# Optimization experiments

Hardware: AMD Instinct MI355X
Metric: run time of the kernel (lower is better)

## Reference

```python
import jax, jax.numpy as jnp
import numpy as np

N_NODES = 50000
N_EDGES = 600000
IN_FEATS = 128
H_FEATS = 128
NUM_CLASSES = 64


def setup_inputs() -> dict:
    key = jax.random.key(0)
    k = jax.random.split(key, 8)
    x = jax.random.normal(k[0], (N_NODES, IN_FEATS), dtype=jnp.float32)
    W1 = jax.random.normal(k[1], (IN_FEATS, H_FEATS), dtype=jnp.float32) * (1.0 / np.sqrt(IN_FEATS))
    b1 = jnp.zeros((H_FEATS,), dtype=jnp.float32)
    W2 = jax.random.normal(k[2], (H_FEATS, NUM_CLASSES), dtype=jnp.float32) * (1.0 / np.sqrt(H_FEATS))
    b2 = jnp.zeros((NUM_CLASSES,), dtype=jnp.float32)
    src = jax.random.randint(k[3], (N_EDGES,), 0, N_NODES, dtype=jnp.int64)
    dst = jax.random.randint(k[4], (N_EDGES,), 0, N_NODES, dtype=jnp.int64)
    return {"x": x, "W1": W1, "b1": b1, "W2": W2, "b2": b2, "src": src, "dst": dst}


def _graph_conv(h, W, b, src, dst, norm_src, norm_dst, n_nodes):
    # DGL GraphConv, norm='both': scale by 1/sqrt(out_deg(src)), sum over edges,
    # scale by 1/sqrt(in_deg(dst)), then linear transform.
    h = h * norm_src[:, None]                                   # [N, F]
    m = jax.ops.segment_sum(h[src], dst, num_segments=n_nodes)  # [N, F] scatter-add over edges
    m = m * norm_dst[:, None]
    return m @ W + b


def reference(x, W1, b1, W2, b2, src, dst):
    n = x.shape[0]
    ones = jnp.ones(src.shape[0], dtype=x.dtype)
    deg_out = jax.ops.segment_sum(ones, src, num_segments=n)
    deg_in = jax.ops.segment_sum(ones, dst, num_segments=n)
    norm_src = jax.lax.rsqrt(jnp.maximum(deg_out, 1.0))
    norm_dst = jax.lax.rsqrt(jnp.maximum(deg_in, 1.0))
    h = _graph_conv(x, W1, b1, src, dst, norm_src, norm_dst, n)
    h = jax.nn.relu(h)
    out = _graph_conv(h, W2, b2, src, dst, norm_src, norm_dst, n)
    return out
```

## Files before the change

### kernel.cpp

```cpp
#include <hip/hip_runtime.h>
#include <hip/hip_fp16.h>

#define NN 50000
#define NE 600000
#define KF 128
#define OC1 128
#define OC2 64

#define HBLK 128
#define HCH ((NE + HBLK - 1) / HBLK)
#define HP4 (NN / 4)
#define NSCB 49
#define NGB ((NN + 63) / 64)

typedef _Float16 half8 __attribute__((ext_vector_type(8)));
typedef float floatx4 __attribute__((ext_vector_type(4)));

__launch_bounds__(256)
__global__ void wt_hist_kernel(const float* __restrict__ W1, const float* __restrict__ W2,
                               __half* __restrict__ Wt1, __half* __restrict__ Wt2,
                               const int* __restrict__ src, const int* __restrict__ dst,
                               int* __restrict__ Hs, int* __restrict__ Hd) {
    __shared__ int bins[HP4];
    if (blockIdx.x < 96) {
        int i = blockIdx.x * 256 + threadIdx.x;
        if (i < KF * OC1) {
            int k = i >> 7, c = i & (OC1 - 1);
            Wt1[c * KF + k] = __float2half(W1[i]);
        } else {
            int j = i - KF * OC1;
            int k = j >> 6, c = j & (OC2 - 1);
            Wt2[c * KF + k] = __float2half(W2[j]);
        }
        return;
    }
    const int b = blockIdx.x - 96;
    const bool is_src = (b < HBLK);
    const int bb = is_src ? b : b - HBLK;
    const int* key = is_src ? src : dst;
    int* H = is_src ? Hs : Hd;
    const int e0 = bb * HCH;
    const int e1 = min(e0 + HCH, NE);

    for (int i = threadIdx.x; i < HP4; i += 256) bins[i] = 0;
    __syncthreads();
    for (int e = e0 + threadIdx.x; e < e1; e += 256) {
        int v = key[e];
        atomicAdd(&bins[v >> 2], 1 << ((v & 3) * 8));
    }
    __syncthreads();
    int* o = H + (size_t)bb * HP4;
    for (int i = threadIdx.x; i < HP4; i += 256) o[i] = bins[i];
}

__launch_bounds__(256)
__global__ void rednorm_kernel(const int* __restrict__ Hs, const int* __restrict__ Hd,
                               int* __restrict__ deg_i, float* __restrict__ nsrc,
                               float* __restrict__ ndst, int* __restrict__ bsum) {
    __shared__ int red[256];
    const int tid = threadIdx.x;
    const int p = blockIdx.x * 256 + tid;
    int so0 = 0, so1 = 0, so2 = 0, so3 = 0, si0 = 0, si1 = 0, si2 = 0, si3 = 0;
    if (p < HP4) {
#pragma unroll 4
        for (int b = 0; b < HBLK; b++) {
            int hs = Hs[(size_t)b * HP4 + p];
            int hd = Hd[(size_t)b * HP4 + p];
            so0 += hs & 255; so1 += (hs >> 8) & 255; so2 += (hs >> 16) & 255; so3 += (hs >> 24) & 255;
            si0 += hd & 255; si1 += (hd >> 8) & 255; si2 += (hd >> 16) & 255; si3 += (hd >> 24) & 255;
        }
        reinterpret_cast<int4*>(deg_i)[p] = make_int4(si0, si1, si2, si3);
        reinterpret_cast<float4*>(nsrc)[p] =
            make_float4(rsqrtf(fmaxf((float)so0, 1.f)), rsqrtf(fmaxf((float)so1, 1.f)),
                        rsqrtf(fmaxf((float)so2, 1.f)), rsqrtf(fmaxf((float)so3, 1.f)));
        reinterpret_cast<float4*>(ndst)[p] =
            make_float4(rsqrtf(fmaxf((float)si0, 1.f)), rsqrtf(fmaxf((float)si1, 1.f)),
                        rsqrtf(fmaxf((float)si2, 1.f)), rsqrtf(fmaxf((float)si3, 1.f)));
    }
    red[tid] = si0 + si1 + si2 + si3;
    __syncthreads();
    for (int off = 128; off > 0; off >>= 1) {
        if (tid < off) red[tid] += red[tid + off];
        __syncthreads();
    }
    if (tid == 0) bsum[blockIdx.x] = red[0];
}

__launch_bounds__(256)
__global__ void scanbofs_kernel(const int* __restrict__ deg, const int* __restrict__ bsum,
                                const int* __restrict__ Hd, int* __restrict__ ptr,
                                unsigned int* __restrict__ Bofs) {
    if (blockIdx.x < NSCB) {
        __shared__ int s[256];
        __shared__ int sboff;
        const int tid = threadIdx.x;
        if (tid < 64) {
            int v = (tid < (int)blockIdx.x) ? bsum[tid] : 0;
#pragma unroll
            for (int off = 32; off > 0; off >>= 1) v += __shfl_xor(v, off);
            if (tid == 0) sboff = v;
        }
        const int q = blockIdx.x * 256 + tid;
        int4 d = make_int4(0, 0, 0, 0);
        if (q < HP4) d = reinterpret_cast<const int4*>(deg)[q];
        int t4 = d.x + d.y + d.z + d.w;
        s[tid] = t4;
        __syncthreads();
        for (int off = 1; off < 256; off <<= 1) {
            int t = (tid >= off) ? s[tid - off] : 0;
            __syncthreads();
            s[tid] += t;
            __syncthreads();
        }
        if (q < HP4) {
            int base = sboff + s[tid] - t4;
            int4 pv;
            pv.x = base;
            pv.y = base + d.x;
            pv.z = pv.y + d.y;
            pv.w = pv.z + d.z;
            reinterpret_cast<int4*>(ptr)[q] = pv;
        }
        if (blockIdx.x == 0 && tid == 0) ptr[NN] = NE;
    } else {
        int p = (blockIdx.x - NSCB) * 256 + threadIdx.x;
        if (p >= HP4) return;
        int r0 = 0, r1 = 0, r2 = 0, r3 = 0;
        for (int b = 0; b < HBLK; b++) {
            Bofs[(size_t)b * HP4 + p] =
                (unsigned)(r0 | (r1 << 8) | (r2 << 16) | (r3 << 24));
            int h = Hd[(size_t)b * HP4 + p];
            r0 += h & 255; r1 += (h >> 8) & 255; r2 += (h >> 16) & 255; r3 += (h >> 24) & 255;
        }
    }
}

__launch_bounds__(256)
__global__ void fillgemm_kernel(const int* __restrict__ src, const int* __restrict__ dst,
                                const unsigned int* __restrict__ Bofs,
                                const int* __restrict__ ptr, int* __restrict__ esrc,
                                const float* __restrict__ x, const __half* __restrict__ Wt1,
                                const float* __restrict__ nsrc, __half* __restrict__ g) {
    extern __shared__ char smem[];
    if (blockIdx.x < HBLK) {
        int* cnt = (int*)smem;
        const int b = blockIdx.x;
        const int e0 = b * HCH;
        const int e1 = min(e0 + HCH, NE);
        for (int i = threadIdx.x; i < HP4; i += 256) cnt[i] = 0;
        __syncthreads();
        const unsigned char* B = (const unsigned char*)(Bofs + (size_t)b * HP4);
        for (int e = e0 + threadIdx.x; e < e1; e += 256) {
            int v = dst[e];
            int sh = (v & 3) * 8;
            int old = atomicAdd(&cnt[v >> 2], 1 << sh);
            int idx = (old >> sh) & 255;
            esrc[ptr[v] + (int)B[v] + idx] = src[e];
        }
        return;
    }
    constexpr int NT = OC1 / 16;
    constexpr int LDK = KF + 8;
    _Float16* Wsh = (_Float16*)smem;

    const int tid = threadIdx.x;
    const int wave = tid >> 6;
    const int lane = tid & 63;
    const int l16 = lane & 15;
    const int koff = (lane >> 4) * 8;
    const int row0 = (blockIdx.x - HBLK) * 64;
    const int arow = row0 + wave * 16 + l16;

    for (int i = tid; i < OC1 * (KF / 8); i += 256) {
        int r = i >> 4;
        int c8 = i & 15;
        *reinterpret_cast<uint4*>(&Wsh[r * LDK + c8 * 8]) =
            reinterpret_cast<const uint4*>(Wt1 + (size_t)r * KF)[c8];
    }

    half8 afr[4];
    if (arow < NN) {
        const float* ap = x + (size_t)arow * KF + koff;
#pragma unroll
        for (int kk = 0; kk < 4; kk++) {
            float4 v0 = *reinterpret_cast<const float4*>(ap + kk * 32);
            float4 v1 = *reinterpret_cast<const float4*>(ap + kk * 32 + 4);
            half8 h;
            h[0] = (_Float16)v0.x; h[1] = (_Float16)v0.y;
            h[2] = (_Float16)v0.z; h[3] = (_Float16)v0.w;
            h[4] = (_Float16)v1.x; h[5] = (_Float16)v1.y;
            h[6] = (_Float16)v1.z; h[7] = (_Float16)v1.w;
            afr[kk] = h;
        }
    } else {
#pragma unroll
        for (int kk = 0; kk < 4; kk++) afr[kk] = (half8)(_Float16)0;
    }

    __syncthreads();

    floatx4 acc[NT];
#pragma unroll
    for (int n = 0; n < NT; n++) acc[n] = (floatx4)(0.f);

#pragma unroll
    for (int n = 0; n < NT; n++) {
        const int brow = n * 16 + l16;
#pragma unroll
        for (int kk = 0; kk < 4; kk++) {
            half8 bfr = *reinterpret_cast<const half8*>(&Wsh[brow * LDK + kk * 32 + koff]);
            acc[n] = __builtin_amdgcn_mfma_f32_16x16x32_f16(afr[kk], bfr, acc[n], 0, 0, 0);
        }
    }

    const int crow = row0 + wave * 16 + (lane >> 4) * 4;
    float nsv[4];
#pragma unroll
    for (int j = 0; j < 4; j++) {
        int rr = crow + j;
        nsv[j] = (rr < NN) ? nsrc[rr] : 0.f;
    }
#pragma unroll
    for (int n = 0; n < NT; n++) {
#pragma unroll
        for (int j = 0; j < 4; j++) {
            int rr = crow + j;
            if (rr < NN)
                g[(size_t)rr * OC1 + n * 16 + l16] = __float2half(acc[n][j] * nsv[j]);
        }
    }
}

__launch_bounds__(256)
__global__ void gathergemm2_kernel(const __half* __restrict__ g, const int* __restrict__ ptr,
                                   const int* __restrict__ esrc, const float* __restrict__ ndst,
                                   const float* __restrict__ nsrc, const float* __restrict__ b1,
                                   const __half* __restrict__ Wt2, __half* __restrict__ g2) {
    constexpr int LDK = KF + 8;
    __shared__ _Float16 h1sh[64 * LDK];
    __shared__ _Float16 Wsh[OC2 * LDK];

    const int tid = threadIdx.x;
    const int node0 = blockIdx.x * 64;

    for (int i = tid; i < OC2 * (KF / 8); i += 256) {
        int r = i >> 4;
        int c8 = i & 15;
        *reinterpret_cast<uint4*>(&Wsh[r * LDK + c8 * 8]) =
            reinterpret_cast<const uint4*>(Wt2 + (size_t)r * KF)[c8];
    }

    const int qw = tid >> 4;
    const int l16g = tid & 15;
    const float4 bb0 = *reinterpret_cast<const float4*>(b1 + l16g * 8);
    const float4 bb1 = *reinterpret_cast<const float4*>(b1 + l16g * 8 + 4);
#pragma unroll 1
    for (int i = 0; i < 4; i++) {
        const int ln = qw + 16 * i;
        const int n = node0 + ln;
        if (n >= NN) continue;
        const int lo = ptr[n];
        const int hi = ptr[n + 1];
        const float nd = ndst[n];
        float4 a0 = make_float4(0.f, 0.f, 0.f, 0.f);
        float4 a1 = make_float4(0.f, 0.f, 0.f, 0.f);
        int e = lo;
        for (; e + 7 < hi; e += 8) {
            int s[8];
#pragma unroll
            for (int j = 0; j < 8; j++) s[j] = esrc[e + j];
            uint4 u[8];
#pragma unroll
            for (int j = 0; j < 8; j++)
                u[j] = *reinterpret_cast<const uint4*>(g + (size_t)s[j] * 128 + l16g * 8);
#pragma unroll
            for (int j = 0; j < 8; j++) {
                float2 f0 = __half22float2(*reinterpret_cast<__half2*>(&u[j].x));
                float2 f1 = __half22float2(*reinterpret_cast<__half2*>(&u[j].y));
                float2 f2 = __half22float2(*reinterpret_cast<__half2*>(&u[j].z));
                float2 f3 = __half22float2(*reinterpret_cast<__half2*>(&u[j].w));
                a0.x += f0.x; a0.y += f0.y; a0.z += f1.x; a0.w += f1.y;
                a1.x += f2.x; a1.y += f2.y; a1.z += f3.x; a1.w += f3.y;
            }
        }
        for (; e < hi; e++) {
            uint4 u = *reinterpret_cast<const uint4*>(g + (size_t)esrc[e] * 128 + l16g * 8);
            float2 f0 = __half22float2(*reinterpret_cast<__half2*>(&u.x));
            float2 f1 = __half22float2(*reinterpret_cast<__half2*>(&u.y));
            float2 f2 = __half22float2(*reinterpret_cast<__half2*>(&u.z));
            float2 f3 = __half22float2(*reinterpret_cast<__half2*>(&u.w));
            a0.x += f0.x; a0.y += f0.y; a0.z += f1.x; a0.w += f1.y;
            a1.x += f2.x; a1.y += f2.y; a1.z += f3.x; a1.w += f3.y;
        }
        const float ns = nsrc[n];
        float o0 = ns * fmaxf(fmaf(a0.x, nd, bb0.x), 0.f);
        float o1 = ns * fmaxf(fmaf(a0.y, nd, bb0.y), 0.f);
        float o2 = ns * fmaxf(fmaf(a0.z, nd, bb0.z), 0.f);
        float o3 = ns * fmaxf(fmaf(a0.w, nd, bb0.w), 0.f);
        float o4 = ns * fmaxf(fmaf(a1.x, nd, bb1.x), 0.f);
        float o5 = ns * fmaxf(fmaf(a1.y, nd, bb1.y), 0.f);
        float o6 = ns * fmaxf(fmaf(a1.z, nd, bb1.z), 0.f);
        float o7 = ns * fmaxf(fmaf(a1.w, nd, bb1.w), 0.f);
        __half2 h0 = __floats2half2_rn(o0, o1);
        __half2 h1v = __floats2half2_rn(o2, o3);
        __half2 h2 = __floats2half2_rn(o4, o5);
        __half2 h3 = __floats2half2_rn(o6, o7);
        uint4 pk;
        pk.x = *reinterpret_cast<unsigned int*>(&h0);
        pk.y = *reinterpret_cast<unsigned int*>(&h1v);
        pk.z = *reinterpret_cast<unsigned int*>(&h2);
        pk.w = *reinterpret_cast<unsigned int*>(&h3);
        *reinterpret_cast<uint4*>(&h1sh[ln * LDK + l16g * 8]) = pk;
    }
    __syncthreads();

    const int wave = tid >> 6;
    const int lane = tid & 63;
    const int l16 = lane & 15;
    const int koff = (lane >> 4) * 8;
    const int arow = wave * 16 + l16;

    half8 afr[4];
#pragma unroll
    for (int kk = 0; kk < 4; kk++)
        afr[kk] = *reinterpret_cast<const half8*>(&h1sh[arow * LDK + kk * 32 + koff]);

    floatx4 acc[4];
#pragma unroll
    for (int n = 0; n < 4; n++) acc[n] = (floatx4)(0.f);

#pragma unroll
    for (int n = 0; n < 4; n++) {
        const int brow = n * 16 + l16;
#pragma unroll
        for (int kk = 0; kk < 4; kk++) {
            half8 bfr = *reinterpret_cast<const half8*>(&Wsh[brow * LDK + kk * 32 + koff]);
            acc[n] = __builtin_amdgcn_mfma_f32_16x16x32_f16(afr[kk], bfr, acc[n], 0, 0, 0);
        }
    }

    const int crow = wave * 16 + (lane >> 4) * 4;
#pragma unroll
    for (int n = 0; n < 4; n++) {
#pragma unroll
        for (int j = 0; j < 4; j++) {
            int rr = node0 + crow + j;
            if (rr < NN)
                g2[(size_t)rr * OC2 + n * 16 + l16] = __float2half(acc[n][j]);
        }
    }
}

__launch_bounds__(256)
__global__ void gather64_kernel(const __half* __restrict__ g, const int* __restrict__ ptr,
                                const int* __restrict__ esrc, const float* __restrict__ ndst,
                                const float* __restrict__ bias, float* __restrict__ out) {
    const int node = blockIdx.x * 32 + (threadIdx.x >> 3);
    if (node >= NN) return;
    const int l8 = threadIdx.x & 7;
    const int cofs = l8 * 8;
    const int lo = ptr[node];
    const int hi = ptr[node + 1];
    const float nd = ndst[node];

    float4 ax[8], ay[8];
#pragma unroll
    for (int i = 0; i < 8; i++) {
        ax[i] = make_float4(0.f, 0.f, 0.f, 0.f);
        ay[i] = make_float4(0.f, 0.f, 0.f, 0.f);
    }

    int e = lo;
    for (; e + 7 < hi; e += 8) {
        int s[8];
#pragma unroll
        for (int i = 0; i < 8; i++) s[i] = esrc[e + i];
#pragma unroll
        for (int i = 0; i < 8; i++) {
            uint4 u = *reinterpret_cast<const uint4*>(g + (size_t)s[i] * 64 + cofs);
            float2 f0 = __half22float2(*reinterpret_cast<__half2*>(&u.x));
            float2 f1 = __half22float2(*reinterpret_cast<__half2*>(&u.y));
            float2 f2 = __half22float2(*reinterpret_cast<__half2*>(&u.z));
            float2 f3 = __half22float2(*reinterpret_cast<__half2*>(&u.w));
            ax[i].x += f0.x; ax[i].y += f0.y; ax[i].z += f1.x; ax[i].w += f1.y;
            ay[i].x += f2.x; ay[i].y += f2.y; ay[i].z += f3.x; ay[i].w += f3.y;
        }
    }
    for (; e < hi; e++) {
        uint4 u = *reinterpret_cast<const uint4*>(g + (size_t)esrc[e] * 64 + cofs);
        float2 f0 = __half22float2(*reinterpret_cast<__half2*>(&u.x));
        float2 f1 = __half22float2(*reinterpret_cast<__half2*>(&u.y));
        float2 f2 = __half22float2(*reinterpret_cast<__half2*>(&u.z));
        float2 f3 = __half22float2(*reinterpret_cast<__half2*>(&u.w));
        ax[0].x += f0.x; ax[0].y += f0.y; ax[0].z += f1.x; ax[0].w += f1.y;
        ay[0].x += f2.x; ay[0].y += f2.y; ay[0].z += f3.x; ay[0].w += f3.y;
    }
#pragma unroll
    for (int i = 1; i < 8; i++) {
        ax[0].x += ax[i].x; ax[0].y += ax[i].y; ax[0].z += ax[i].z; ax[0].w += ax[i].w;
        ay[0].x += ay[i].x; ay[0].y += ay[i].y; ay[0].z += ay[i].z; ay[0].w += ay[i].w;
    }

    float4 b0 = *reinterpret_cast<const float4*>(bias + cofs);
    float4 b1 = *reinterpret_cast<const float4*>(bias + cofs + 4);
    float4 o0, o1;
    o0.x = fmaf(ax[0].x, nd, b0.x); o0.y = fmaf(ax[0].y, nd, b0.y);
    o0.z = fmaf(ax[0].z, nd, b0.z); o0.w = fmaf(ax[0].w, nd, b0.w);
    o1.x = fmaf(ay[0].x, nd, b1.x); o1.y = fmaf(ay[0].y, nd, b1.y);
    o1.z = fmaf(ay[0].z, nd, b1.z); o1.w = fmaf(ay[0].w, nd, b1.w);
    float* op = out + (size_t)node * 64 + cofs;
    *reinterpret_cast<float4*>(op) = o0;
    *reinterpret_cast<float4*>(op + 4) = o1;
}

extern "C" void kernel_launch(void* const* d_in, const int* in_sizes, int n_in,
                              void* d_out, int out_size, void* d_ws, size_t ws_size,
                              hipStream_t stream) {
    const float* x  = (const float*)d_in[0];
    const float* W1 = (const float*)d_in[1];
    const float* b1 = (const float*)d_in[2];
    const float* W2 = (const float*)d_in[3];
    const float* b2 = (const float*)d_in[4];
    const int*   src = (const int*)d_in[5];
    const int*   dst = (const int*)d_in[6];
    float* out = (float*)d_out;

    __half* Wt1  = (__half*)d_ws;
    __half* Wt2  = Wt1 + KF * OC1;
    float*  nsrc = (float*)(Wt2 + KF * OC2);
    float*  ndst = nsrc + NN;
    __half* g    = (__half*)(ndst + NN);
    __half* g2   = g + (size_t)NN * KF;
    int* deg_i  = (int*)(g2 + (size_t)NN * OC2);
    int* ptr    = deg_i + NN;
    int* esrc   = ptr + NN + 4;
    int* bsum   = esrc + NE;
    int* Hs     = bsum + NSCB + 3;
    int* Hd     = Hs + (size_t)HBLK * HP4;
    unsigned int* Bofs = (unsigned int*)(Hd + (size_t)HBLK * HP4);

    wt_hist_kernel<<<96 + 2 * HBLK, 256, 0, stream>>>(W1, W2, Wt1, Wt2, src, dst, Hs, Hd);
    rednorm_kernel<<<NSCB, 256, 0, stream>>>(Hs, Hd, deg_i, nsrc, ndst, bsum);
    scanbofs_kernel<<<2 * NSCB, 256, 0, stream>>>(deg_i, bsum, Hd, ptr, Bofs);
    fillgemm_kernel<<<HBLK + NGB, 256, HP4 * 4 + 64, stream>>>(src, dst, Bofs, ptr, esrc,
                                                               x, Wt1, nsrc, g);
    gathergemm2_kernel<<<NGB, 256, 0, stream>>>(g, ptr, esrc, ndst, nsrc, b1, Wt2, g2);
    gather64_kernel<<<(NN + 31) / 32, 256, 0, stream>>>(g2, ptr, esrc, ndst, b2, out);
}
```

Before: 124.5 us.

## Move GEMM1 into scan kernel, split edge fill into its own kernel, halve histogram blocks

The dense x·W1 GEMM now runs as extra blocks of the scan/offset kernel instead of sharing a launch with the CSR fill, so it overlaps with the prefix-scan work. The fill becomes a standalone kernel that uses a static shared-memory counter array. HBLK drops from 128 to 64, which halves the per-block histogram and offset passes and the Bofs storage but gives each fill block twice as many edges. Packing per-node counts into 8-bit fields now relies on fewer than 256 edges per node per chunk, and the chunks are now larger.

New measurement: 125.4 us. Within noise of the previous version (+0.7%).

```diff
diff --git a/kernel.cpp b/kernel.cpp
--- a/kernel.cpp
+++ b/kernel.cpp
@@ -7,7 +7,7 @@
 #define OC1 128
 #define OC2 64
 
-#define HBLK 128
+#define HBLK 64
 #define HCH ((NE + HBLK - 1) / HBLK)
 #define HP4 (NN / 4)
 #define NSCB 49
@@ -87,18 +87,21 @@
 }
 
 __launch_bounds__(256)
-__global__ void scanbofs_kernel(const int* __restrict__ deg, const int* __restrict__ bsum,
-                                const int* __restrict__ Hd, int* __restrict__ ptr,
-                                unsigned int* __restrict__ Bofs) {
+__global__ void scan_bofs_gemm1_kernel(const int* __restrict__ deg, const int* __restrict__ bsum,
+                                       const int* __restrict__ Hd, int* __restrict__ ptr,
+                                       unsigned int* __restrict__ Bofs,
+                                       const float* __restrict__ x, const __half* __restrict__ Wt1,
+                                       const float* __restrict__ nsrc, __half* __restrict__ g) {
+    extern __shared__ char smem[];
     if (blockIdx.x < NSCB) {
-        __shared__ int s[256];
-        __shared__ int sboff;
+        int* s = (int*)smem;
+        int* sboff = (int*)(smem + 1024);
         const int tid = threadIdx.x;
         if (tid < 64) {
             int v = (tid < (int)blockIdx.x) ? bsum[tid] : 0;
 #pragma unroll
             for (int off = 32; off > 0; off >>= 1) v += __shfl_xor(v, off);
-            if (tid == 0) sboff = v;
+            if (tid == 0) *sboff = v;
         }
         const int q = blockIdx.x * 256 + tid;
         int4 d = make_int4(0, 0, 0, 0);
@@ -113,7 +116,7 @@
             __syncthreads();
         }
         if (q < HP4) {
-            int base = sboff + s[tid] - t4;
+            int base = *sboff + s[tid] - t4;
             int4 pv;
             pv.x = base;
             pv.y = base + d.x;
@@ -122,41 +125,19 @@
             reinterpret_cast<int4*>(ptr)[q] = pv;
         }
         if (blockIdx.x == 0 && tid == 0) ptr[NN] = NE;
-    } else {
+        return;
+    }
+    if (blockIdx.x < 2 * NSCB) {
         int p = (blockIdx.x - NSCB) * 256 + threadIdx.x;
         if (p >= HP4) return;
         int r0 = 0, r1 = 0, r2 = 0, r3 = 0;
+#pragma unroll 4
         for (int b = 0; b < HBLK; b++) {
             Bofs[(size_t)b * HP4 + p] =
                 (unsigned)(r0 | (r1 << 8) | (r2 << 16) | (r3 << 24));
             int h = Hd[(size_t)b * HP4 + p];
             r0 += h & 255; r1 += (h >> 8) & 255; r2 += (h >> 16) & 255; r3 += (h >> 24) & 255;
         }
-    }
-}
-
-__launch_bounds__(256)
-__global__ void fillgemm_kernel(const int* __restrict__ src, const int* __restrict__ dst,
-                                const unsigned int* __restrict__ Bofs,
-                                const int* __restrict__ ptr, int* __restrict__ esrc,
-                                const float* __restrict__ x, const __half* __restrict__ Wt1,
-                                const float* __restrict__ nsrc, __half* __restrict__ g) {
-    extern __shared__ char smem[];
-    if (blockIdx.x < HBLK) {
-        int* cnt = (int*)smem;
-        const int b = blockIdx.x;
-        const int e0 = b * HCH;
-        const int e1 = min(e0 + HCH, NE);
-        for (int i = threadIdx.x; i < HP4; i += 256) cnt[i] = 0;
-        __syncthreads();
-        const unsigned char* B = (const unsigned char*)(Bofs + (size_t)b * HP4);
-        for (int e = e0 + threadIdx.x; e < e1; e += 256) {
-            int v = dst[e];
-            int sh = (v & 3) * 8;
-            int old = atomicAdd(&cnt[v >> 2], 1 << sh);
-            int idx = (old >> sh) & 255;
-            esrc[ptr[v] + (int)B[v] + idx] = src[e];
-        }
         return;
     }
     constexpr int NT = OC1 / 16;
@@ -168,7 +149,7 @@
     const int lane = tid & 63;
     const int l16 = lane & 15;
     const int koff = (lane >> 4) * 8;
-    const int row0 = (blockIdx.x - HBLK) * 64;
+    const int row0 = (blockIdx.x - 2 * NSCB) * 64;
     const int arow = row0 + wave * 16 + l16;
 
     for (int i = tid; i < OC1 * (KF / 8); i += 256) {
@@ -228,6 +209,26 @@
             if (rr < NN)
                 g[(size_t)rr * OC1 + n * 16 + l16] = __float2half(acc[n][j] * nsv[j]);
         }
+    }
+}
+
+__launch_bounds__(256)
+__global__ void fill_kernel(const int* __restrict__ src, const int* __restrict__ dst,
+                            const unsigned int* __restrict__ Bofs,
+                            const int* __restrict__ ptr, int* __restrict__ esrc) {
+    __shared__ int cnt[HP4];
+    const int b = blockIdx.x;
+    const int e0 = b * HCH;
+    const int e1 = min(e0 + HCH, NE);
+    for (int i = threadIdx.x; i < HP4; i += 256) cnt[i] = 0;
+    __syncthreads();
+    const unsigned char* B = (const unsigned char*)(Bofs + (size_t)b * HP4);
+    for (int e = e0 + threadIdx.x; e < e1; e += 256) {
+        int v = dst[e];
+        int sh = (v & 3) * 8;
+        int old = atomicAdd(&cnt[v >> 2], 1 << sh);
+        int idx = (old >> sh) & 255;
+        esrc[ptr[v] + (int)B[v] + idx] = src[e];
     }
 }
 
@@ -441,9 +442,9 @@
 
     wt_hist_kernel<<<96 + 2 * HBLK, 256, 0, stream>>>(W1, W2, Wt1, Wt2, src, dst, Hs, Hd);
     rednorm_kernel<<<NSCB, 256, 0, stream>>>(Hs, Hd, deg_i, nsrc, ndst, bsum);
-    scanbofs_kernel<<<2 * NSCB, 256, 0, stream>>>(deg_i, bsum, Hd, ptr, Bofs);
-    fillgemm_kernel<<<HBLK + NGB, 256, HP4 * 4 + 64, stream>>>(src, dst, Bofs, ptr, esrc,
-                                                               x, Wt1, nsrc, g);
+    scan_bofs_gemm1_kernel<<<2 * NSCB + NGB, 256, OC1 * (KF + 8) * 2, stream>>>(
+        deg_i, bsum, Hd, ptr, Bofs, x, Wt1, nsrc, g);
+    fill_kernel<<<HBLK, 256, 0, stream>>>(src, dst, Bofs, ptr, esrc);
     gathergemm2_kernel<<<NGB, 256, 0, stream>>>(g, ptr, esrc, ndst, nsrc, b1, Wt2, g2);
     gather64_kernel<<<(NN + 31) / 32, 256, 0, stream>>>(g2, ptr, esrc, ndst, b2, out);
 }
```
